# Kernel tuning notes

Measured on AMD Instinct MI355X. Metric: run time of the kernel, lower is better.

The kernel has to match this reference:

```python
import jax, jax.numpy as jnp
import numpy as np

N_NODES = 50000
N_EDGES = 800000
IN_C, HID_C, OUT_C = 256, 256, 128


def setup_inputs() -> dict:
    key = jax.random.key(0)
    k1, k2, k3, k4 = jax.random.split(key, 4)
    x = jax.random.normal(k1, (N_NODES, IN_C), dtype=jnp.float32)
    edge_index = jax.random.randint(k2, (2, N_EDGES), 0, N_NODES, dtype=jnp.int64)
    W1 = jax.random.normal(k3, (IN_C, HID_C), dtype=jnp.float32) / np.sqrt(IN_C)
    b1 = jnp.zeros((HID_C,), dtype=jnp.float32)
    W2 = jax.random.normal(k4, (HID_C, OUT_C), dtype=jnp.float32) / np.sqrt(HID_C)
    b2 = jnp.zeros((OUT_C,), dtype=jnp.float32)
    return {"x": x, "edge_index": edge_index, "W1": W1, "b1": b1, "W2": W2, "b2": b2}


def _gcn_norm(edge_index, n_nodes):
    # Add self-loops, compute symmetric normalization D^-1/2 (A+I) D^-1/2 (PyG GCNConv default).
    loop = jnp.arange(n_nodes, dtype=edge_index.dtype)
    src = jnp.concatenate([edge_index[0], loop])  # [E+N]
    dst = jnp.concatenate([edge_index[1], loop])  # [E+N]
    deg = jax.ops.segment_sum(jnp.ones_like(dst, dtype=jnp.float32), dst, num_segments=n_nodes)
    dinv = jnp.where(deg > 0, 1.0 / jnp.sqrt(deg), 0.0)
    norm = dinv[src] * dinv[dst]  # [E+N]
    return src, dst, norm


def _gcn_conv(x, src, dst, norm, W, b, n_nodes):
    h = x @ W                                  # [N, out] dense GEMM first (PyG order)
    msg = h[src] * norm[:, None]               # gather + scale: [E+N, out]
    out = jax.ops.segment_sum(msg, dst, num_segments=n_nodes)  # scatter-add
    return out + b


def reference(x, edge_index, W1, b1, W2, b2):
    n = x.shape[0]
    src, dst, norm = _gcn_norm(edge_index, n)
    h = _gcn_conv(x, src, dst, norm, W1, b1, n)
    h = jax.nn.relu(h)
    # dropout is identity in eval mode
    return _gcn_conv(h, src, dst, norm, W2, b2, n)
```

## Files before the change

### kernel.cpp

```cpp
#include <hip/hip_runtime.h>
#include <cstdint>
#include <cstddef>


static constexpr int CH1 = 256;
static constexpr int CH2 = 128;

typedef __attribute__((ext_vector_type(8))) short bf16x8;
typedef __attribute__((ext_vector_type(4))) float f32x4;
typedef __attribute__((ext_vector_type(8))) unsigned short u16x8;

__device__ inline unsigned short f2bf(float f) {
  unsigned u = __builtin_bit_cast(unsigned, f);
  return (unsigned short)((u + 0x7fffu + ((u >> 16) & 1u)) >> 16);
}
__device__ inline float lo16(unsigned u) { return __builtin_bit_cast(float, u << 16); }
__device__ inline float hi16(unsigned u) { return __builtin_bit_cast(float, u & 0xffff0000u); }

__device__ inline void gload16(const void* g, void* l) {
  __builtin_amdgcn_global_load_lds(
      (const __attribute__((address_space(1))) unsigned int*)g,
      (__attribute__((address_space(3))) unsigned int*)l, 16, 0, 0);
}


__global__ void k_init_deg(int* __restrict__ deg, int n, int* __restrict__ flag) {
  int i = blockIdx.x * blockDim.x + threadIdx.x;
  if (i < n) deg[i] = 0;
  if (i == 0) *flag = 0;
}

__global__ void k_detect_i32(const unsigned int* __restrict__ w, int nwords,
                             int* __restrict__ flag) {
  int i = blockIdx.x * blockDim.x + threadIdx.x;
  if (i < nwords && (i & 1) && w[i] != 0u) *flag = 1;
}

__global__ void k_cvt_deg(const void* __restrict__ raw, int* __restrict__ e32,
                          int* __restrict__ deg, int E, const int* __restrict__ flag) {
  int i = blockIdx.x * blockDim.x + threadIdx.x;
  if (i >= 2 * E) return;
  int v = (*flag) ? ((const int*)raw)[i] : (int)((const long long*)raw)[i];
  e32[i] = v;
  if (i >= E) atomicAdd(&deg[v], 1);
}

__global__ __launch_bounds__(256) void k_chunk_sum(const int* __restrict__ deg,
                                                   int* __restrict__ bsum, int N) {
  __shared__ int sh[256];
  int i = blockIdx.x * 256 + threadIdx.x;
  sh[threadIdx.x] = (i < N) ? deg[i] : 0;
  __syncthreads();
  for (int off = 128; off > 0; off >>= 1) {
    if (threadIdx.x < (unsigned)off) sh[threadIdx.x] += sh[threadIdx.x + off];
    __syncthreads();
  }
  if (threadIdx.x == 0) bsum[blockIdx.x] = sh[0];
}

__global__ __launch_bounds__(256) void k_scan_bsums(int* __restrict__ bsum, int nb) {
  __shared__ int sh[256];
  int t = threadIdx.x;
  int v = (t < nb) ? bsum[t] : 0;
  sh[t] = v;
  __syncthreads();
  for (int off = 1; off < 256; off <<= 1) {
    int add = (t >= off) ? sh[t - off] : 0;
    __syncthreads();
    sh[t] += add;
    __syncthreads();
  }
  if (t < nb) bsum[t] = sh[t] - v;
}

__global__ __launch_bounds__(256) void k_chunk_scan(
    const int* __restrict__ deg, const int* __restrict__ bsum,
    int* __restrict__ rowstart, int* __restrict__ cursor,
    float* __restrict__ dinv, int N, int E) {
  __shared__ int sh[256];
  int t = threadIdx.x;
  int i = blockIdx.x * 256 + t;
  int d = (i < N) ? deg[i] : 0;
  sh[t] = d;
  __syncthreads();
  for (int off = 1; off < 256; off <<= 1) {
    int add = (t >= off) ? sh[t - off] : 0;
    __syncthreads();
    sh[t] += add;
    __syncthreads();
  }
  if (i < N) {
    int rs = bsum[blockIdx.x] + sh[t] - d;
    rowstart[i] = rs;
    cursor[i]   = rs;
    dinv[i] = rsqrtf((float)(d + 1));
  }
  if (i == 0) rowstart[N] = E;
}

__global__ void k_fill(const int* __restrict__ src, const int* __restrict__ dst,
                       int* __restrict__ cursor, int* __restrict__ csr, int E) {
  int e = blockIdx.x * blockDim.x + threadIdx.x;
  if (e < E) {
    int pos = atomicAdd(&cursor[dst[e]], 1);
    csr[pos] = src[e];
  }
}

__global__ void k_prep(const float4* __restrict__ x, u16x8* __restrict__ xo, int n8x,
                       const float* __restrict__ W1, unsigned short* __restrict__ w1t,
                       int Ka, int Na,
                       const float* __restrict__ W2, unsigned short* __restrict__ w2t,
                       int Kb, int Nb) {
  int i = blockIdx.x * blockDim.x + threadIdx.x;
  if (i < n8x) {
    float4 a = x[i * 2], b = x[i * 2 + 1];
    u16x8 p;
    p[0] = f2bf(a.x); p[1] = f2bf(a.y); p[2] = f2bf(a.z); p[3] = f2bf(a.w);
    p[4] = f2bf(b.x); p[5] = f2bf(b.y); p[6] = f2bf(b.z); p[7] = f2bf(b.w);
    xo[i] = p;
    return;
  }
  i -= n8x;
  if (i < Ka * Na) {
    int k = i / Na, n = i - k * Na;
    w1t[(size_t)n * Ka + k] = f2bf(W1[i]);
    return;
  }
  i -= Ka * Na;
  if (i < Kb * Nb) {
    int k = i / Nb, n = i - k * Nb;
    w2t[(size_t)n * Kb + k] = f2bf(W2[i]);
  }
}

template <int BN>
__global__ __launch_bounds__(256) void k_gemm_mfma(
    const unsigned short* __restrict__ A, const unsigned short* __restrict__ Bt,
    const float* __restrict__ dinv, unsigned short* __restrict__ Co, int M, int K) {
  constexpr int BM = 64, BK = 32;
  constexpr int NF = BN / 64;
  constexpr int ASZ = BM * BK;
  constexpr int BSZ = BN * BK;
  __shared__ unsigned short lds[2][ASZ + BSZ];
  const int t = threadIdx.x;
  const int w = t >> 6, l = t & 63;
  const int m0 = blockIdx.x * BM;
  const int lr = l & 15, lk = l >> 4;

  auto stage = [&](int buf, int k0) {
    unsigned short* base = lds[buf];
    {
      int row = t >> 2, p = t & 3;
      int s = p ^ ((row >> 1) & 3);
      int gm = m0 + row; if (gm >= M) gm = M - 1;
      gload16(A + (size_t)gm * K + k0 + s * 8, base + (size_t)row * BK + p * 8);
    }
    for (int i = t; i < BN * 4; i += 256) {
      int n = i >> 2, p = i & 3;
      int s = p ^ ((n >> 1) & 3);
      gload16(Bt + (size_t)n * K + k0 + s * 8, base + ASZ + (size_t)n * BK + p * 8);
    }
  };

  f32x4 acc[4][NF];
#pragma unroll
  for (int a = 0; a < 4; ++a)
#pragma unroll
    for (int b = 0; b < NF; ++b) acc[a][b] = (f32x4){0.f, 0.f, 0.f, 0.f};

  stage(0, 0);
  __syncthreads();
  const int nsteps = K / BK;
  for (int ks = 0; ks < nsteps; ++ks) {
    int cur = ks & 1;
    if (ks + 1 < nsteps) stage(cur ^ 1, (ks + 1) * BK);
    const unsigned short* base = lds[cur];
    bf16x8 ah[4], bh[NF];
#pragma unroll
    for (int fm = 0; fm < 4; ++fm) {
      int row = fm * 16 + lr;
      int p = lk ^ ((row >> 1) & 3);
      ah[fm] = *(const bf16x8*)(base + row * BK + p * 8);
    }
#pragma unroll
    for (int fb = 0; fb < NF; ++fb) {
      int n = w * (BN / 4) + fb * 16 + lr;
      int p = lk ^ ((n >> 1) & 3);
      bh[fb] = *(const bf16x8*)(base + ASZ + n * BK + p * 8);
    }
#pragma unroll
    for (int fm = 0; fm < 4; ++fm)
#pragma unroll
      for (int fb = 0; fb < NF; ++fb)
        acc[fm][fb] = __builtin_amdgcn_mfma_f32_16x16x32_bf16(ah[fm], bh[fb], acc[fm][fb], 0, 0, 0);
    __syncthreads();
  }
#pragma unroll
  for (int fm = 0; fm < 4; ++fm)
#pragma unroll
    for (int r = 0; r < 4; ++r) {
      int row = m0 + fm * 16 + lk * 4 + r;
      if (row < M) {
        float dv = dinv[row];
#pragma unroll
        for (int fb = 0; fb < NF; ++fb) {
          int col = w * (BN / 4) + fb * 16 + lr;
          size_t o = ((size_t)(col >> 6) * M + row) * 64 + (col & 63);
          Co[o] = f2bf(dv * acc[fm][fb][r]);
        }
      }
    }
}

template <int C, int MODE>
__global__ __launch_bounds__(256) void k_agg_slice(
    const int* __restrict__ rowstart, const int* __restrict__ csr,
    const float* __restrict__ dinv, const unsigned short* __restrict__ gS,
    const float* __restrict__ bias, float* __restrict__ out,
    unsigned short* __restrict__ of1, int N) {
  constexpr int NSL = C / 64;
  constexpr int DUP = 8 / NSL;
  const int x = blockIdx.x & 7;
  const int slice = x & (NSL - 1);
  const int dup = x >> (NSL == 4 ? 2 : 1);
  const int nb = ((int)blockIdx.x >> 3) * DUP + dup;
  const int v = nb * 8 + ((int)threadIdx.x >> 5);
  if (v >= N) return;
  const int ln = threadIdx.x & 31;
  const int sub = ln >> 3;
  const int l8 = ln & 7;
  const unsigned short* __restrict__ base = gS + (size_t)slice * N * 64 + l8 * 8;

  const unsigned selL = 0x00003f80u;
  const unsigned selH = 0x3f800000u;
  float acc[8] = {0.f, 0.f, 0.f, 0.f, 0.f, 0.f, 0.f, 0.f};
#define DOT2(k, word, sel) \
  asm("v_dot2_f32_bf16 %0, %1, %2, %0" : "+v"(acc[k]) : "v"(word), "v"(sel));
#define ACC8(u)                 \
  { DOT2(0, (u).x, selL) DOT2(1, (u).x, selH)  \
    DOT2(2, (u).y, selL) DOT2(3, (u).y, selH)  \
    DOT2(4, (u).z, selL) DOT2(5, (u).z, selH)  \
    DOT2(6, (u).w, selL) DOT2(7, (u).w, selH) }

  const int end = rowstart[v + 1];
  int j = rowstart[v] + sub;
  for (; j + 4 < end; j += 8) {
    int s0 = csr[j], s1 = csr[j + 4];
    uint4 r0 = *(const uint4*)(base + (size_t)s0 * 64);
    uint4 r1 = *(const uint4*)(base + (size_t)s1 * 64);
    ACC8(r0) ACC8(r1)
  }
  if (j < end) {
    uint4 r = *(const uint4*)(base + (size_t)csr[j] * 64);
    ACC8(r)
  }
#pragma unroll
  for (int k = 0; k < 8; ++k) {
    acc[k] += __shfl_xor(acc[k], 8, 32);
    acc[k] += __shfl_xor(acc[k], 16, 32);
  }
  if (sub != 0) return;
  {
    uint4 r = *(const uint4*)(base + (size_t)v * 64);
    ACC8(r)
  }
#undef ACC8
#undef DOT2
  const float dv = dinv[v];
  const int c0 = slice * 64 + l8 * 8;
  const float4 bA = *(const float4*)(bias + c0);
  const float4 bB = *(const float4*)(bias + c0 + 4);
  float o[8];
  o[0] = dv * acc[0] + bA.x; o[1] = dv * acc[1] + bA.y;
  o[2] = dv * acc[2] + bA.z; o[3] = dv * acc[3] + bA.w;
  o[4] = dv * acc[4] + bB.x; o[5] = dv * acc[5] + bB.y;
  o[6] = dv * acc[6] + bB.z; o[7] = dv * acc[7] + bB.w;
  if constexpr (MODE == 1) {
    u16x8 p;
#pragma unroll
    for (int k = 0; k < 8; ++k) p[k] = f2bf(fmaxf(o[k], 0.f));
    *(u16x8*)(of1 + (size_t)v * C + c0) = p;
  } else {
    *(float4*)(out + (size_t)v * C + c0) = make_float4(o[0], o[1], o[2], o[3]);
    *(float4*)(out + (size_t)v * C + c0 + 4) = make_float4(o[4], o[5], o[6], o[7]);
  }
}


extern "C" void kernel_launch(void* const* d_in, const int* in_sizes, int n_in,
                              void* d_out, int out_size, void* d_ws, size_t ws_size,
                              hipStream_t stream) {
  const float* x  = (const float*)d_in[0];
  const void*  ei = d_in[1];
  const float* W1 = (const float*)d_in[2];
  const float* b1 = (const float*)d_in[3];
  const float* W2 = (const float*)d_in[4];
  const float* b2 = (const float*)d_in[5];
  float* out = (float*)d_out;

  const int N = in_sizes[0] / CH1;
  const int E = in_sizes[1] / 2;

  char* w = (char*)d_ws;
  size_t off = 0;
  auto alloc = [&](size_t bytes) -> void* {
    void* p = w + off;
    off += (bytes + 255) & ~(size_t)255;
    return p;
  };
  int*   deg      = (int*)alloc((size_t)N * 4);
  int*   flag     = (int*)alloc(256);
  int*   e32      = (int*)alloc((size_t)2 * E * 4);
  int*   rowstart = (int*)alloc((size_t)(N + 1) * 4);
  int*   cursor   = (int*)alloc((size_t)N * 4);
  int*   bsum     = (int*)alloc(256 * 4);
  int*   csr      = (int*)alloc((size_t)E * 4);
  float* dinv     = (float*)alloc((size_t)N * 4);
  unsigned short* xh  = (unsigned short*)alloc((size_t)N * CH1 * 2);
  unsigned short* g1S = (unsigned short*)alloc((size_t)N * CH1 * 2);
  unsigned short* g2S = (unsigned short*)alloc((size_t)N * CH2 * 2);
  unsigned short* w1t = (unsigned short*)alloc((size_t)CH1 * CH1 * 2);
  unsigned short* w2t = (unsigned short*)alloc((size_t)CH1 * CH2 * 2);

  const int* srcI = e32;
  const int* dstI = e32 + E;

  dim3 blk(256);
  auto cdiv = [](long long a, long long b) { return (int)((a + b - 1) / b); };
  const int nchunks = cdiv(N, 256);
  const int nodeblk8 = cdiv(N, 8);
  const int n8x = N * CH1 / 8;

  k_init_deg<<<cdiv(N, 256), blk, 0, stream>>>(deg, N, flag);
  k_detect_i32<<<cdiv(2LL * E, 256), blk, 0, stream>>>((const unsigned int*)ei, 2 * E, flag);
  k_cvt_deg<<<cdiv(2LL * E, 256), blk, 0, stream>>>(ei, e32, deg, E, flag);
  k_chunk_sum<<<nchunks, blk, 0, stream>>>(deg, bsum, N);
  k_scan_bsums<<<1, blk, 0, stream>>>(bsum, nchunks);
  k_chunk_scan<<<nchunks, blk, 0, stream>>>(deg, bsum, rowstart, cursor, dinv, N, E);
  k_fill<<<cdiv(E, 256), blk, 0, stream>>>(srcI, dstI, cursor, csr, E);

  k_prep<<<cdiv((long long)n8x + CH1 * CH1 + CH1 * CH2, 256), blk, 0, stream>>>(
      (const float4*)x, (u16x8*)xh, n8x, W1, w1t, CH1, CH1, W2, w2t, CH1, CH2);

  k_gemm_mfma<CH1><<<cdiv(N, 64), blk, 0, stream>>>(xh, w1t, dinv, g1S, N, CH1);
  k_agg_slice<CH1, 1><<<cdiv(nodeblk8, 2) * 8, blk, 0, stream>>>(
      rowstart, csr, dinv, g1S, b1, nullptr, xh, N);

  k_gemm_mfma<CH2><<<cdiv(N, 64), blk, 0, stream>>>(xh, w2t, dinv, g2S, N, CH1);
  k_agg_slice<CH2, 0><<<cdiv(nodeblk8, 4) * 8, blk, 0, stream>>>(
      rowstart, csr, dinv, g2S, b2, out, nullptr, N);
}
```

Before: 244.9 us.

## Enlarge GEMM tile to 128 rows with 8 waves; grid-stride aggregation kernels

The MFMA GEMM now uses 512-thread blocks covering 128 rows, with waves split 2x4 over M and N, so each staged B tile serves twice as many rows. The two aggregation kernels become persistent grid-stride loops over node blocks with a fixed grid of 2048 blocks, and the bias load is hoisted out of the per-node work. This aims to cut B reloads and block launch overhead, at the cost of fewer GEMM blocks and possible load imbalance in the fixed aggregation grid.

```diff
diff --git a/kernel.cpp b/kernel.cpp
--- a/kernel.cpp
+++ b/kernel.cpp
@@ -14,8 +14,6 @@
   unsigned u = __builtin_bit_cast(unsigned, f);
   return (unsigned short)((u + 0x7fffu + ((u >> 16) & 1u)) >> 16);
 }
-__device__ inline float lo16(unsigned u) { return __builtin_bit_cast(float, u << 16); }
-__device__ inline float hi16(unsigned u) { return __builtin_bit_cast(float, u & 0xffff0000u); }
 
 __device__ inline void gload16(const void* g, void* l) {
   __builtin_amdgcn_global_load_lds(
@@ -135,16 +133,17 @@
 }
 
 template <int BN>
-__global__ __launch_bounds__(256) void k_gemm_mfma(
+__global__ __launch_bounds__(512) void k_gemm_mfma(
     const unsigned short* __restrict__ A, const unsigned short* __restrict__ Bt,
     const float* __restrict__ dinv, unsigned short* __restrict__ Co, int M, int K) {
-  constexpr int BM = 64, BK = 32;
+  constexpr int BM = 128, BK = 32;
   constexpr int NF = BN / 64;
   constexpr int ASZ = BM * BK;
   constexpr int BSZ = BN * BK;
   __shared__ unsigned short lds[2][ASZ + BSZ];
   const int t = threadIdx.x;
   const int w = t >> 6, l = t & 63;
+  const int wm = w >> 2, wn = w & 3;
   const int m0 = blockIdx.x * BM;
   const int lr = l & 15, lk = l >> 4;
 
@@ -156,7 +155,7 @@
       int gm = m0 + row; if (gm >= M) gm = M - 1;
       gload16(A + (size_t)gm * K + k0 + s * 8, base + (size_t)row * BK + p * 8);
     }
-    for (int i = t; i < BN * 4; i += 256) {
+    for (int i = t; i < BN * 4; i += 512) {
       int n = i >> 2, p = i & 3;
       int s = p ^ ((n >> 1) & 3);
       gload16(Bt + (size_t)n * K + k0 + s * 8, base + ASZ + (size_t)n * BK + p * 8);
@@ -179,13 +178,13 @@
     bf16x8 ah[4], bh[NF];
 #pragma unroll
     for (int fm = 0; fm < 4; ++fm) {
-      int row = fm * 16 + lr;
+      int row = wm * 64 + fm * 16 + lr;
       int p = lk ^ ((row >> 1) & 3);
       ah[fm] = *(const bf16x8*)(base + row * BK + p * 8);
     }
 #pragma unroll
     for (int fb = 0; fb < NF; ++fb) {
-      int n = w * (BN / 4) + fb * 16 + lr;
+      int n = wn * (BN / 4) + fb * 16 + lr;
       int p = lk ^ ((n >> 1) & 3);
       bh[fb] = *(const bf16x8*)(base + ASZ + n * BK + p * 8);
     }
@@ -200,12 +199,12 @@
   for (int fm = 0; fm < 4; ++fm)
 #pragma unroll
     for (int r = 0; r < 4; ++r) {
-      int row = m0 + fm * 16 + lk * 4 + r;
+      int row = m0 + wm * 64 + fm * 16 + lk * 4 + r;
       if (row < M) {
         float dv = dinv[row];
 #pragma unroll
         for (int fb = 0; fb < NF; ++fb) {
-          int col = w * (BN / 4) + fb * 16 + lr;
+          int col = wn * (BN / 4) + fb * 16 + lr;
           size_t o = ((size_t)(col >> 6) * M + row) * 64 + (col & 63);
           Co[o] = f2bf(dv * acc[fm][fb][r]);
         }
@@ -218,23 +217,23 @@
     const int* __restrict__ rowstart, const int* __restrict__ csr,
     const float* __restrict__ dinv, const unsigned short* __restrict__ gS,
     const float* __restrict__ bias, float* __restrict__ out,
-    unsigned short* __restrict__ of1, int N) {
+    unsigned short* __restrict__ of1, int N, int nodeblocks) {
   constexpr int NSL = C / 64;
   constexpr int DUP = 8 / NSL;
   const int x = blockIdx.x & 7;
   const int slice = x & (NSL - 1);
   const int dup = x >> (NSL == 4 ? 2 : 1);
-  const int nb = ((int)blockIdx.x >> 3) * DUP + dup;
-  const int v = nb * 8 + ((int)threadIdx.x >> 5);
-  if (v >= N) return;
+  const int bstride = ((int)gridDim.x >> 3) * DUP;
   const int ln = threadIdx.x & 31;
   const int sub = ln >> 3;
   const int l8 = ln & 7;
   const unsigned short* __restrict__ base = gS + (size_t)slice * N * 64 + l8 * 8;
+  const int c0 = slice * 64 + l8 * 8;
+  const float4 bA = *(const float4*)(bias + c0);
+  const float4 bB = *(const float4*)(bias + c0 + 4);
 
   const unsigned selL = 0x00003f80u;
   const unsigned selH = 0x3f800000u;
-  float acc[8] = {0.f, 0.f, 0.f, 0.f, 0.f, 0.f, 0.f, 0.f};
 #define DOT2(k, word, sel) \
   asm("v_dot2_f32_bf16 %0, %1, %2, %0" : "+v"(acc[k]) : "v"(word), "v"(sel));
 #define ACC8(u)                 \
@@ -243,48 +242,51 @@
     DOT2(4, (u).z, selL) DOT2(5, (u).z, selH)  \
     DOT2(6, (u).w, selL) DOT2(7, (u).w, selH) }
 
-  const int end = rowstart[v + 1];
-  int j = rowstart[v] + sub;
-  for (; j + 4 < end; j += 8) {
-    int s0 = csr[j], s1 = csr[j + 4];
-    uint4 r0 = *(const uint4*)(base + (size_t)s0 * 64);
-    uint4 r1 = *(const uint4*)(base + (size_t)s1 * 64);
-    ACC8(r0) ACC8(r1)
-  }
-  if (j < end) {
-    uint4 r = *(const uint4*)(base + (size_t)csr[j] * 64);
-    ACC8(r)
-  }
-#pragma unroll
-  for (int k = 0; k < 8; ++k) {
-    acc[k] += __shfl_xor(acc[k], 8, 32);
-    acc[k] += __shfl_xor(acc[k], 16, 32);
-  }
-  if (sub != 0) return;
-  {
-    uint4 r = *(const uint4*)(base + (size_t)v * 64);
-    ACC8(r)
+  for (int nb = ((int)blockIdx.x >> 3) * DUP + dup; nb < nodeblocks; nb += bstride) {
+    const int v = nb * 8 + ((int)threadIdx.x >> 5);
+    if (v >= N) continue;
+    float acc[8] = {0.f, 0.f, 0.f, 0.f, 0.f, 0.f, 0.f, 0.f};
+    const int end = rowstart[v + 1];
+    int j = rowstart[v] + sub;
+    for (; j + 4 < end; j += 8) {
+      int s0 = csr[j], s1 = csr[j + 4];
+      uint4 r0 = *(const uint4*)(base + (size_t)s0 * 64);
+      uint4 r1 = *(const uint4*)(base + (size_t)s1 * 64);
+      ACC8(r0) ACC8(r1)
+    }
+    if (j < end) {
+      uint4 r = *(const uint4*)(base + (size_t)csr[j] * 64);
+      ACC8(r)
+    }
+#pragma unroll
+    for (int k = 0; k < 8; ++k) {
+      acc[k] += __shfl_xor(acc[k], 8, 32);
+      acc[k] += __shfl_xor(acc[k], 16, 32);
+    }
+    if (sub == 0) {
+      {
+        uint4 r = *(const uint4*)(base + (size_t)v * 64);
+        ACC8(r)
+      }
+      const float dv = dinv[v];
+      float o[8];
+      o[0] = dv * acc[0] + bA.x; o[1] = dv * acc[1] + bA.y;
+      o[2] = dv * acc[2] + bA.z; o[3] = dv * acc[3] + bA.w;
+      o[4] = dv * acc[4] + bB.x; o[5] = dv * acc[5] + bB.y;
+      o[6] = dv * acc[6] + bB.z; o[7] = dv * acc[7] + bB.w;
+      if constexpr (MODE == 1) {
+        u16x8 p;
+#pragma unroll
+        for (int k = 0; k < 8; ++k) p[k] = f2bf(fmaxf(o[k], 0.f));
+        *(u16x8*)(of1 + (size_t)v * C + c0) = p;
+      } else {
+        *(float4*)(out + (size_t)v * C + c0) = make_float4(o[0], o[1], o[2], o[3]);
+        *(float4*)(out + (size_t)v * C + c0 + 4) = make_float4(o[4], o[5], o[6], o[7]);
+      }
+    }
   }
 #undef ACC8
 #undef DOT2
-  const float dv = dinv[v];
-  const int c0 = slice * 64 + l8 * 8;
-  const float4 bA = *(const float4*)(bias + c0);
-  const float4 bB = *(const float4*)(bias + c0 + 4);
-  float o[8];
-  o[0] = dv * acc[0] + bA.x; o[1] = dv * acc[1] + bA.y;
-  o[2] = dv * acc[2] + bA.z; o[3] = dv * acc[3] + bA.w;
-  o[4] = dv * acc[4] + bB.x; o[5] = dv * acc[5] + bB.y;
-  o[6] = dv * acc[6] + bB.z; o[7] = dv * acc[7] + bB.w;
-  if constexpr (MODE == 1) {
-    u16x8 p;
-#pragma unroll
-    for (int k = 0; k < 8; ++k) p[k] = f2bf(fmaxf(o[k], 0.f));
-    *(u16x8*)(of1 + (size_t)v * C + c0) = p;
-  } else {
-    *(float4*)(out + (size_t)v * C + c0) = make_float4(o[0], o[1], o[2], o[3]);
-    *(float4*)(out + (size_t)v * C + c0 + 4) = make_float4(o[4], o[5], o[6], o[7]);
-  }
 }
 
 
@@ -326,11 +328,12 @@
   const int* srcI = e32;
   const int* dstI = e32 + E;
 
-  dim3 blk(256);
+  dim3 blk(256), blk512(512);
   auto cdiv = [](long long a, long long b) { return (int)((a + b - 1) / b); };
   const int nchunks = cdiv(N, 256);
-  const int nodeblk8 = cdiv(N, 8);
+  const int nodeblocks = cdiv(N, 8);
   const int n8x = N * CH1 / 8;
+  const int AGG_GRID = 2048;
 
   k_init_deg<<<cdiv(N, 256), blk, 0, stream>>>(deg, N, flag);
   k_detect_i32<<<cdiv(2LL * E, 256), blk, 0, stream>>>((const unsigned int*)ei, 2 * E, flag);
@@ -343,11 +346,11 @@
   k_prep<<<cdiv((long long)n8x + CH1 * CH1 + CH1 * CH2, 256), blk, 0, stream>>>(
       (const float4*)x, (u16x8*)xh, n8x, W1, w1t, CH1, CH1, W2, w2t, CH1, CH2);
 
-  k_gemm_mfma<CH1><<<cdiv(N, 64), blk, 0, stream>>>(xh, w1t, dinv, g1S, N, CH1);
-  k_agg_slice<CH1, 1><<<cdiv(nodeblk8, 2) * 8, blk, 0, stream>>>(
-      rowstart, csr, dinv, g1S, b1, nullptr, xh, N);
-
-  k_gemm_mfma<CH2><<<cdiv(N, 64), blk, 0, stream>>>(xh, w2t, dinv, g2S, N, CH1);
-  k_agg_slice<CH2, 0><<<cdiv(nodeblk8, 4) * 8, blk, 0, stream>>>(
-      rowstart, csr, dinv, g2S, b2, out, nullptr, N);
-}
+  k_gemm_mfma<CH1><<<cdiv(N, 128), blk512, 0, stream>>>(xh, w1t, dinv, g1S, N, CH1);
+  k_agg_slice<CH1, 1><<<AGG_GRID, blk, 0, stream>>>(
+      rowstart, csr, dinv, g1S, b1, nullptr, xh, N, nodeblocks);
+
+  k_gemm_mfma<CH2><<<cdiv(N, 128), blk512, 0, stream>>>(xh, w2t, dinv, g2S, N, CH1);
+  k_agg_slice<CH2, 0><<<AGG_GRID, blk, 0, stream>>>(
+      rowstart, csr, dinv, g2S, b2, out, nullptr, N, nodeblocks);
+}
```

After: 225.9 us (median of 2 runs). -7.8%, faster.
